# Performance work log

Hardware: AMD Instinct MI355X
Metric: run time of the kernel (lower is better)

Reference implementation:

```python
import jax, jax.numpy as jnp
import numpy as np

G = 128          # voxel grid extent per axis
B = G + 2        # key base, allows coords in [-1, G] after +1 shift
N_PTS = 100000
C_IN = 32
C_OUT = 32


def _key(c):
    # c: [..., 3] int32 voxel coords in [-1, G]; unique linear key per voxel
    return ((c[..., 0] + 1) * B + (c[..., 1] + 1)) * B + (c[..., 2] + 1)


def setup_inputs() -> dict:
    key = jax.random.key(0)
    k1, k2, k3 = jax.random.split(key, 3)
    positions = jax.random.randint(k1, (N_PTS, 3), 0, G, dtype=jnp.int32)
    features = jax.random.normal(k2, (N_PTS, C_IN), dtype=jnp.float32)
    # per-offset filter matrices, [K^3, Cin, Cout], fan-in style init
    weight = jax.random.normal(k3, (27, C_IN, C_OUT), dtype=jnp.float32) * (1.0 / np.sqrt(27 * C_IN))
    return {"features": features, "positions": positions, "weight": weight}


def reference(features, positions, weight):
    # Submanifold sparse conv: output at the same sparse positions as input.
    # For each of the 27 kernel offsets, hash-lookup the neighbor voxel,
    # gather its feature (or 0 if absent), matmul with the per-offset filter,
    # accumulate. use_bias=False, normalize=False, voxel_size=1.0, offset=0.
    n = features.shape[0]
    keys = _key(positions)                      # [N]
    order = jnp.argsort(keys)
    sk = keys[order]                            # sorted keys (hash table)

    ax = jnp.arange(-1, 2, dtype=jnp.int32)
    off = jnp.stack(jnp.meshgrid(ax, ax, ax, indexing="ij"), axis=-1).reshape(27, 3)

    qk = _key(positions[None, :, :] + off[:, None, :])          # [27, N]
    pos_idx = jnp.clip(jnp.searchsorted(sk, qk), 0, n - 1)      # [27, N]
    match = sk[pos_idx] == qk                                   # neighbor exists?
    gidx = order[pos_idx]                                       # original index of neighbor

    gf = jnp.where(match[..., None], features[gidx], 0.0)       # [27, N, Cin] gather
    out = jnp.einsum("onc,ocd->nd", gf, weight)                 # scatter-accumulate via reduce over o
    return out
```

## Files before the change

kernel.cpp:

```cpp
#include <hip/hip_runtime.h>


#define GRID_B 130
#define GRID_CELLS 2197000
#define BM_WORDS 68704
#define C 32
#define NTHR 512
#define PTS 64
#define CAP 24
#define ROWS_CAP 192

__global__ void build_grid_kernel(const int* __restrict__ pos,
                                  int* __restrict__ grid,
                                  unsigned int* __restrict__ bm, int n) {
    int i = blockIdx.x * blockDim.x + threadIdx.x;
    if (i >= n) return;
    int x = pos[3 * i + 0] + 1;
    int y = pos[3 * i + 1] + 1;
    int z = pos[3 * i + 2] + 1;
    int key = (x * GRID_B + y) * GRID_B + z;
    atomicMax(&grid[key], n - i);
    atomicOr(&bm[key >> 5], 1u << (key & 31));
}

__global__ __launch_bounds__(NTHR)
void conv_kernel(const float* __restrict__ feat,
                 const int* __restrict__ pos,
                 const float* __restrict__ w,
                 const int* __restrict__ grid,
                 const unsigned int* __restrict__ bm,
                 float* __restrict__ out, int n) {
    __shared__ int   s_cnt[27];
    __shared__ int   s_seg[27];
    __shared__ int   s_total;
    __shared__ int   s_list[27][CAP];
    __shared__ int   s_rep[PTS];
    __shared__ int   s_jidx[ROWS_CAP];
    __shared__ int   s_pos[PTS * 3];
    __shared__ __align__(16) float s_rows[ROWS_CAP][C];
    __shared__ __align__(16) float s_acc[PTS][C];

    const int tid = threadIdx.x;
    const int pt_base = blockIdx.x * PTS;

    if (tid < 27) s_cnt[tid] = 0;
    for (int u = tid; u < PTS * 3; u += NTHR) {
        int g = pt_base * 3 + u;
        if (g < n * 3) s_pos[u] = pos[g];
    }
    __syncthreads();

    for (int t = tid; t < PTS * 9; t += NTHR) {
        int pl = t / 9;
        int xy = t - pl * 9;
        if (pt_base + pl < n) {
            int dx = xy / 3;
            int dy = xy - dx * 3;
            int x0 = s_pos[pl * 3 + 0] + dx;
            int y0 = s_pos[pl * 3 + 1] + dy;
            int k0 = (x0 * GRID_B + y0) * GRID_B + s_pos[pl * 3 + 2];
            unsigned int w0 = bm[(k0 >> 5)];
            unsigned int w1 = bm[(k0 >> 5) + 1];
            unsigned int bits =
                (unsigned int)((((unsigned long long)w1 << 32) | w0) >> (k0 & 31)) & 7u;
            int obase = xy * 3;
            if (xy == 4) {
                s_rep[pl] = k0 + 1;
                bits &= 5u;
            }
            while (bits) {
                int oz = __ffs(bits) - 1;
                bits &= bits - 1;
                int slot = atomicAdd(&s_cnt[obase + oz], 1);
                if (slot < CAP) s_list[obase + oz][slot] = (pl << 22) | (k0 + oz);
            }
        }
    }
    __syncthreads();

    if (tid < 64) {
        int o = tid;
        int c = (o < 27 && o != 13) ? min(s_cnt[o], CAP) : 0;
        int x = c;
        #pragma unroll
        for (int d = 1; d < 32; d <<= 1) {
            int y = __shfl_up(x, d, 64);
            if (tid >= d) x += y;
        }
        if (o < 27) s_seg[o] = PTS + x - c;
        if (o == 26) s_total = PTS + x;
    }
    __syncthreads();

    for (int t = tid; t < 27 * CAP + PTS; t += NTHR) {
        if (t < 27 * CAP) {
            int o = t / CAP;
            int slot = t - o * CAP;
            if (o != 13 && slot < min(s_cnt[o], CAP)) {
                int f = s_seg[o] + slot;
                if (f < ROWS_CAP)
                    s_jidx[f] = n - grid[s_list[o][slot] & 0x3FFFFF];
            }
        } else {
            int pl = t - 27 * CAP;
            s_jidx[pl] = (pt_base + pl < n) ? (n - grid[s_rep[pl]]) : 0;
        }
    }
    __syncthreads();

    {
        int totc = min(s_total, ROWS_CAP);
        int lane = tid & 63, wv = tid >> 6;
        int nI = (totc + 7) >> 3;
        for (int i = wv; i < nI; i += 8) {
            int f = (i << 3) + (lane >> 3);
            int j = s_jidx[min(f, totc - 1)];
            const float* g = feat + (size_t)j * C + ((lane & 7) << 2);
            __builtin_amdgcn_global_load_lds(
                (const __attribute__((address_space(1))) unsigned int*)g,
                (__attribute__((address_space(3))) unsigned int*)(&s_rows[i << 3][0]),
                16, 0, 0);
        }
    }
    asm volatile("s_waitcnt vmcnt(0)" ::: "memory");
    __syncthreads();

    {
        const int hw16 = tid >> 5;
        const int cout = tid & 31;
        const int cnt13 = min(PTS, n - pt_base);
        float wreg[32];
        #pragma unroll
        for (int c = 0; c < 32; ++c) wreg[c] = w[13 * 1024 + c * 32 + cout];
        for (int e = hw16; e < cnt13; e += 16) {
            const float4* R = (const float4*)(&s_rows[e][0]);
            float acc = 0.0f;
            #pragma unroll
            for (int k = 0; k < 8; ++k) {
                float4 rv = R[k];
                acc = fmaf(rv.x, wreg[4 * k + 0], acc);
                acc = fmaf(rv.y, wreg[4 * k + 1], acc);
                acc = fmaf(rv.z, wreg[4 * k + 2], acc);
                acc = fmaf(rv.w, wreg[4 * k + 3], acc);
            }
            s_acc[e][cout] = acc;
        }
    }
    __syncthreads();

    {
        const int wv = tid >> 6;
        const int lane = tid & 63;
        const int cout = lane & 31;
        const int half = lane >> 5;
        for (int o = wv; o < 27; o += 8) {
            if (o == 13) continue;
            int cnt = min(s_cnt[o], CAP);
            if (cnt == 0) continue;
            int seg = s_seg[o];
            float wreg[32];
            #pragma unroll
            for (int c = 0; c < 32; ++c) wreg[c] = w[o * 1024 + c * 32 + cout];
            for (int e = half; e < cnt; e += 2) {
                int f = seg + e;
                if (f >= ROWS_CAP) break;
                int pl = ((unsigned int)s_list[o][e]) >> 22;
                const float4* R = (const float4*)(&s_rows[f][0]);
                float acc = 0.0f;
                #pragma unroll
                for (int k = 0; k < 8; ++k) {
                    float4 rv = R[k];
                    acc = fmaf(rv.x, wreg[4 * k + 0], acc);
                    acc = fmaf(rv.y, wreg[4 * k + 1], acc);
                    acc = fmaf(rv.z, wreg[4 * k + 2], acc);
                    acc = fmaf(rv.w, wreg[4 * k + 3], acc);
                }
                atomicAdd(&s_acc[pl][cout], acc);
            }
        }
    }
    __syncthreads();

    {
        const int base = pt_base * C;
        const int lim = n * C - base;
        for (int u = tid; u < PTS * C && u < lim; u += NTHR)
            out[base + u] = s_acc[u >> 5][u & 31];
    }
}

extern "C" void kernel_launch(void* const* d_in, const int* in_sizes, int n_in,
                              void* d_out, int out_size, void* d_ws, size_t ws_size,
                              hipStream_t stream) {
    const float* features = (const float*)d_in[0];
    const int*   positions = (const int*)d_in[1];
    const float* weight = (const float*)d_in[2];
    float* out = (float*)d_out;
    const int n = in_sizes[0] / C;

    int* grid = (int*)d_ws;
    unsigned int* bm = (unsigned int*)(grid + GRID_CELLS);
    hipMemsetAsync(d_ws, 0, (size_t)(GRID_CELLS + BM_WORDS) * sizeof(int), stream);

    build_grid_kernel<<<(n + 255) / 256, 256, 0, stream>>>(positions, grid, bm, n);

    conv_kernel<<<(n + PTS - 1) / PTS, NTHR, 0, stream>>>(features, positions, weight,
                                                          grid, bm, out, n);
}
```

Before: 120.1 us.

## Use persistent 1024-thread blocks with per-offset weight-resident half-waves

Converts the conv kernel into a persistent grid of 512 blocks of 1024 threads that loop over point tiles. Each half-wave owns one kernel offset and keeps its 32 weight values in registers across all tiles, so weights are no longer reloaded per tile. Neighbor slots are assigned directly through a flat atomic counter, which removes the prefix-scan and the separate grid-lookup pass. The costs are more shared atomics on the accumulator, load imbalance because each offset is handled by a single half-wave, and only 512 blocks to cover the device.

```diff
diff --git a/kernel.cpp b/kernel.cpp
--- a/kernel.cpp
+++ b/kernel.cpp
@@ -5,10 +5,11 @@
 #define GRID_CELLS 2197000
 #define BM_WORDS 68704
 #define C 32
-#define NTHR 512
+#define NTHR 1024
 #define PTS 64
 #define CAP 24
-#define ROWS_CAP 192
+#define ROWS_CAP 208
+#define NBLK 512
 
 __global__ void build_grid_kernel(const int* __restrict__ pos,
                                   int* __restrict__ grid,
@@ -23,7 +24,7 @@
     atomicOr(&bm[key >> 5], 1u << (key & 31));
 }
 
-__global__ __launch_bounds__(NTHR)
+__global__ __launch_bounds__(NTHR, 4)
 void conv_kernel(const float* __restrict__ feat,
                  const int* __restrict__ pos,
                  const float* __restrict__ w,
@@ -31,140 +32,120 @@
                  const unsigned int* __restrict__ bm,
                  float* __restrict__ out, int n) {
     __shared__ int   s_cnt[27];
-    __shared__ int   s_seg[27];
-    __shared__ int   s_total;
+    __shared__ int   s_flat;
     __shared__ int   s_list[27][CAP];
-    __shared__ int   s_rep[PTS];
-    __shared__ int   s_jidx[ROWS_CAP];
+    __shared__ int   s_key[ROWS_CAP];
     __shared__ int   s_pos[PTS * 3];
     __shared__ __align__(16) float s_rows[ROWS_CAP][C];
     __shared__ __align__(16) float s_acc[PTS][C];
 
     const int tid = threadIdx.x;
-    const int pt_base = blockIdx.x * PTS;
+    const int hw = tid >> 5;
+    const int cout = tid & 31;
+    const int lane = tid & 63;
+    const int wv = tid >> 6;
 
-    if (tid < 27) s_cnt[tid] = 0;
-    for (int u = tid; u < PTS * 3; u += NTHR) {
-        int g = pt_base * 3 + u;
-        if (g < n * 3) s_pos[u] = pos[g];
-    }
-    __syncthreads();
+    const int o_own = (hw < 27 && hw != 13) ? hw : 13;
+    float wreg[32];
+    #pragma unroll
+    for (int c = 0; c < 32; ++c) wreg[c] = w[o_own * 1024 + c * 32 + cout];
 
-    for (int t = tid; t < PTS * 9; t += NTHR) {
-        int pl = t / 9;
-        int xy = t - pl * 9;
-        if (pt_base + pl < n) {
-            int dx = xy / 3;
-            int dy = xy - dx * 3;
-            int x0 = s_pos[pl * 3 + 0] + dx;
-            int y0 = s_pos[pl * 3 + 1] + dy;
-            int k0 = (x0 * GRID_B + y0) * GRID_B + s_pos[pl * 3 + 2];
-            unsigned int w0 = bm[(k0 >> 5)];
-            unsigned int w1 = bm[(k0 >> 5) + 1];
-            unsigned int bits =
-                (unsigned int)((((unsigned long long)w1 << 32) | w0) >> (k0 & 31)) & 7u;
-            int obase = xy * 3;
-            if (xy == 4) {
-                s_rep[pl] = k0 + 1;
-                bits &= 5u;
-            }
-            while (bits) {
-                int oz = __ffs(bits) - 1;
-                bits &= bits - 1;
-                int slot = atomicAdd(&s_cnt[obase + oz], 1);
-                if (slot < CAP) s_list[obase + oz][slot] = (pl << 22) | (k0 + oz);
+    const int ntiles = (n + PTS - 1) / PTS;
+    for (int tile = blockIdx.x; tile < ntiles; tile += NBLK) {
+        const int pt_base = tile * PTS;
+
+        if (tid < 27) s_cnt[tid] = 0;
+        if (tid == 31) s_flat = PTS;
+        if (tid >= 32 && tid < 32 + PTS * 3) {
+            int u = tid - 32;
+            int g = pt_base * 3 + u;
+            if (g < n * 3) s_pos[u] = pos[g];
+        }
+        {
+            float* a = &s_acc[0][0];
+            for (int u = tid; u < PTS * C; u += NTHR) a[u] = 0.0f;
+        }
+        __syncthreads();
+
+        if (tid < PTS * 9) {
+            int pl = tid / 9;
+            int xy = tid - pl * 9;
+            if (pt_base + pl < n) {
+                int dx = xy / 3;
+                int dy = xy - dx * 3;
+                int x0 = s_pos[pl * 3 + 0] + dx;
+                int y0 = s_pos[pl * 3 + 1] + dy;
+                int k0 = (x0 * GRID_B + y0) * GRID_B + s_pos[pl * 3 + 2];
+                unsigned int w0 = bm[(k0 >> 5)];
+                unsigned int w1 = bm[(k0 >> 5) + 1];
+                unsigned int bits =
+                    (unsigned int)((((unsigned long long)w1 << 32) | w0) >> (k0 & 31)) & 7u;
+                int obase = xy * 3;
+                if (xy == 4) {
+                    s_key[pl] = k0 + 1;
+                    bits &= 5u;
+                }
+                while (bits) {
+                    int oz = __ffs(bits) - 1;
+                    bits &= bits - 1;
+                    int o = obase + oz;
+                    int slot = atomicAdd(&s_cnt[o], 1);
+                    if (slot < CAP) {
+                        int f = atomicAdd(&s_flat, 1);
+                        if (f < ROWS_CAP) {
+                            s_key[f] = k0 + oz;
+                            s_list[o][slot] = (pl << 8) | f;
+                        } else {
+                            s_list[o][slot] = -1;
+                        }
+                    }
+                }
+            } else if (xy == 4) {
+                s_key[pl] = 0;
             }
         }
-    }
-    __syncthreads();
+        __syncthreads();
 
-    if (tid < 64) {
-        int o = tid;
-        int c = (o < 27 && o != 13) ? min(s_cnt[o], CAP) : 0;
-        int x = c;
-        #pragma unroll
-        for (int d = 1; d < 32; d <<= 1) {
-            int y = __shfl_up(x, d, 64);
-            if (tid >= d) x += y;
+        {
+            int totc = min(s_flat, ROWS_CAP);
+            int nI = (totc + 7) >> 3;
+            for (int i = wv; i < nI; i += 16) {
+                int f = (i << 3) + (lane >> 3);
+                int key = s_key[min(f, totc - 1)];
+                int j = min(n - grid[key], n - 1);
+                const float* g = feat + (size_t)j * C + ((lane & 7) << 2);
+                __builtin_amdgcn_global_load_lds(
+                    (const __attribute__((address_space(1))) unsigned int*)g,
+                    (__attribute__((address_space(3))) unsigned int*)(&s_rows[i << 3][0]),
+                    16, 0, 0);
+            }
         }
-        if (o < 27) s_seg[o] = PTS + x - c;
-        if (o == 26) s_total = PTS + x;
-    }
-    __syncthreads();
+        asm volatile("s_waitcnt vmcnt(0)" ::: "memory");
+        __syncthreads();
 
-    for (int t = tid; t < 27 * CAP + PTS; t += NTHR) {
-        if (t < 27 * CAP) {
-            int o = t / CAP;
-            int slot = t - o * CAP;
-            if (o != 13 && slot < min(s_cnt[o], CAP)) {
-                int f = s_seg[o] + slot;
-                if (f < ROWS_CAP)
-                    s_jidx[f] = n - grid[s_list[o][slot] & 0x3FFFFF];
+        if (o_own == 13) {
+            int ch = (hw == 13) ? 0 : (hw - 26);
+            int cnt13 = min(PTS, n - pt_base);
+            for (int e = ch; e < cnt13; e += 6) {
+                const float4* R = (const float4*)(&s_rows[e][0]);
+                float acc = 0.0f;
+                #pragma unroll
+                for (int k = 0; k < 8; ++k) {
+                    float4 rv = R[k];
+                    acc = fmaf(rv.x, wreg[4 * k + 0], acc);
+                    acc = fmaf(rv.y, wreg[4 * k + 1], acc);
+                    acc = fmaf(rv.z, wreg[4 * k + 2], acc);
+                    acc = fmaf(rv.w, wreg[4 * k + 3], acc);
+                }
+                atomicAdd(&s_acc[e][cout], acc);
             }
         } else {
-            int pl = t - 27 * CAP;
-            s_jidx[pl] = (pt_base + pl < n) ? (n - grid[s_rep[pl]]) : 0;
-        }
-    }
-    __syncthreads();
-
-    {
-        int totc = min(s_total, ROWS_CAP);
-        int lane = tid & 63, wv = tid >> 6;
-        int nI = (totc + 7) >> 3;
-        for (int i = wv; i < nI; i += 8) {
-            int f = (i << 3) + (lane >> 3);
-            int j = s_jidx[min(f, totc - 1)];
-            const float* g = feat + (size_t)j * C + ((lane & 7) << 2);
-            __builtin_amdgcn_global_load_lds(
-                (const __attribute__((address_space(1))) unsigned int*)g,
-                (__attribute__((address_space(3))) unsigned int*)(&s_rows[i << 3][0]),
-                16, 0, 0);
-        }
-    }
-    asm volatile("s_waitcnt vmcnt(0)" ::: "memory");
-    __syncthreads();
-
-    {
-        const int hw16 = tid >> 5;
-        const int cout = tid & 31;
-        const int cnt13 = min(PTS, n - pt_base);
-        float wreg[32];
-        #pragma unroll
-        for (int c = 0; c < 32; ++c) wreg[c] = w[13 * 1024 + c * 32 + cout];
-        for (int e = hw16; e < cnt13; e += 16) {
-            const float4* R = (const float4*)(&s_rows[e][0]);
-            float acc = 0.0f;
-            #pragma unroll
-            for (int k = 0; k < 8; ++k) {
-                float4 rv = R[k];
-                acc = fmaf(rv.x, wreg[4 * k + 0], acc);
-                acc = fmaf(rv.y, wreg[4 * k + 1], acc);
-                acc = fmaf(rv.z, wreg[4 * k + 2], acc);
-                acc = fmaf(rv.w, wreg[4 * k + 3], acc);
-            }
-            s_acc[e][cout] = acc;
-        }
-    }
-    __syncthreads();
-
-    {
-        const int wv = tid >> 6;
-        const int lane = tid & 63;
-        const int cout = lane & 31;
-        const int half = lane >> 5;
-        for (int o = wv; o < 27; o += 8) {
-            if (o == 13) continue;
-            int cnt = min(s_cnt[o], CAP);
-            if (cnt == 0) continue;
-            int seg = s_seg[o];
-            float wreg[32];
-            #pragma unroll
-            for (int c = 0; c < 32; ++c) wreg[c] = w[o * 1024 + c * 32 + cout];
-            for (int e = half; e < cnt; e += 2) {
-                int f = seg + e;
-                if (f >= ROWS_CAP) break;
-                int pl = ((unsigned int)s_list[o][e]) >> 22;
+            int cnt = min(s_cnt[o_own], CAP);
+            for (int e = 0; e < cnt; ++e) {
+                int pk = s_list[o_own][e];
+                if (pk < 0) continue;
+                int pl = pk >> 8;
+                int f = pk & 255;
                 const float4* R = (const float4*)(&s_rows[f][0]);
                 float acc = 0.0f;
                 #pragma unroll
@@ -178,14 +159,15 @@
                 atomicAdd(&s_acc[pl][cout], acc);
             }
         }
-    }
-    __syncthreads();
+        __syncthreads();
 
-    {
-        const int base = pt_base * C;
-        const int lim = n * C - base;
-        for (int u = tid; u < PTS * C && u < lim; u += NTHR)
-            out[base + u] = s_acc[u >> 5][u & 31];
+        {
+            const int base = pt_base * C;
+            const int lim = n * C - base;
+            for (int u = tid; u < PTS * C && u < lim; u += NTHR)
+                out[base + u] = s_acc[u >> 5][u & 31];
+        }
+        __syncthreads();
     }
 }
 
@@ -204,6 +186,6 @@
 
     build_grid_kernel<<<(n + 255) / 256, 256, 0, stream>>>(positions, grid, bm, n);
 
-    conv_kernel<<<(n + PTS - 1) / PTS, NTHR, 0, stream>>>(features, positions, weight,
-                                                          grid, bm, out, n);
+    conv_kernel<<<NBLK, NTHR, 0, stream>>>(features, positions, weight,
+                                           grid, bm, out, n);
 }
```

Result: slower. 153.0 us (+27.3%).

## Replace dense voxel index grid with open-addressing hash table

Applied to the files above, without the earlier changes.

Swaps the dense 2.2M-cell index grid for a 2^18-slot linear-probing hash table (key and value arrays) built with atomicCAS, keeping the occupancy bitmap for existence tests. This shrinks the memset from about 9 MB to about 2.3 MB and cuts the memory footprint of the lookup structure. In exchange, build and lookup take probe loops with divergent, dependent global loads. Key 0 is used as the empty marker, which is safe only because shifted coordinates never produce key 0 for valid points.

```diff
diff --git a/kernel.cpp b/kernel.cpp
--- a/kernel.cpp
+++ b/kernel.cpp
@@ -2,7 +2,9 @@
 
 
 #define GRID_B 130
-#define GRID_CELLS 2197000
+#define HBITS 18
+#define HSIZE (1 << HBITS)
+#define HMASK (HSIZE - 1)
 #define BM_WORDS 68704
 #define C 32
 #define NTHR 512
@@ -10,8 +12,13 @@
 #define CAP 24
 #define ROWS_CAP 192
 
-__global__ void build_grid_kernel(const int* __restrict__ pos,
-                                  int* __restrict__ grid,
+__device__ __forceinline__ unsigned hash_slot(int key) {
+    return ((unsigned)key * 2654435761u) >> (32 - HBITS);
+}
+
+__global__ void build_hash_kernel(const int* __restrict__ pos,
+                                  unsigned int* __restrict__ hkey,
+                                  unsigned int* __restrict__ hval,
                                   unsigned int* __restrict__ bm, int n) {
     int i = blockIdx.x * blockDim.x + threadIdx.x;
     if (i >= n) return;
@@ -19,15 +26,32 @@
     int y = pos[3 * i + 1] + 1;
     int z = pos[3 * i + 2] + 1;
     int key = (x * GRID_B + y) * GRID_B + z;
-    atomicMax(&grid[key], n - i);
     atomicOr(&bm[key >> 5], 1u << (key & 31));
+    unsigned h = hash_slot(key);
+    while (true) {
+        unsigned old = atomicCAS(&hkey[h], 0u, (unsigned)key);
+        if (old == 0u || old == (unsigned)key) {
+            atomicMax(&hval[h], (unsigned)(n - i));
+            break;
+        }
+        h = (h + 1) & HMASK;
+    }
+}
+
+__device__ __forceinline__ int hash_lookup(const unsigned int* __restrict__ hkey,
+                                           const unsigned int* __restrict__ hval,
+                                           int key, int n) {
+    unsigned h = hash_slot(key);
+    while (hkey[h] != (unsigned)key) h = (h + 1) & HMASK;
+    return n - (int)hval[h];
 }
 
 __global__ __launch_bounds__(NTHR)
 void conv_kernel(const float* __restrict__ feat,
                  const int* __restrict__ pos,
                  const float* __restrict__ w,
-                 const int* __restrict__ grid,
+                 const unsigned int* __restrict__ hkey,
+                 const unsigned int* __restrict__ hval,
                  const unsigned int* __restrict__ bm,
                  float* __restrict__ out, int n) {
     __shared__ int   s_cnt[27];
@@ -99,11 +123,12 @@
             if (o != 13 && slot < min(s_cnt[o], CAP)) {
                 int f = s_seg[o] + slot;
                 if (f < ROWS_CAP)
-                    s_jidx[f] = n - grid[s_list[o][slot] & 0x3FFFFF];
+                    s_jidx[f] = hash_lookup(hkey, hval, s_list[o][slot] & 0x3FFFFF, n);
             }
         } else {
             int pl = t - 27 * CAP;
-            s_jidx[pl] = (pt_base + pl < n) ? (n - grid[s_rep[pl]]) : 0;
+            s_jidx[pl] = (pt_base + pl < n)
+                       ? hash_lookup(hkey, hval, s_rep[pl], n) : 0;
         }
     }
     __syncthreads();
@@ -198,12 +223,13 @@
     float* out = (float*)d_out;
     const int n = in_sizes[0] / C;
 
-    int* grid = (int*)d_ws;
-    unsigned int* bm = (unsigned int*)(grid + GRID_CELLS);
-    hipMemsetAsync(d_ws, 0, (size_t)(GRID_CELLS + BM_WORDS) * sizeof(int), stream);
-
-    build_grid_kernel<<<(n + 255) / 256, 256, 0, stream>>>(positions, grid, bm, n);
+    unsigned int* hkey = (unsigned int*)d_ws;
+    unsigned int* hval = hkey + HSIZE;
+    unsigned int* bm   = hkey + 2 * HSIZE;
+    hipMemsetAsync(d_ws, 0, (size_t)(2 * HSIZE + BM_WORDS) * sizeof(int), stream);
+
+    build_hash_kernel<<<(n + 255) / 256, 256, 0, stream>>>(positions, hkey, hval, bm, n);
 
     conv_kernel<<<(n + PTS - 1) / PTS, NTHR, 0, stream>>>(features, positions, weight,
-                                                          grid, bm, out, n);
-}
+                                                          hkey, hval, bm, out, n);
+}
```

New measurement: 133.3 us. +10.9%, slower.
